# Performance work log

Hardware: AMD Instinct MI355X
Metric: run time of the kernel (lower is better)

## Reference

```python
import jax, jax.numpy as jnp
import numpy as np

NUM_GROUPS = 32
EPS = 1e-6


def group_norm(x, gamma, beta):
    # x: [b, c, h, w]
    b, c, h, w = x.shape
    xg = x.reshape(b, NUM_GROUPS, c // NUM_GROUPS, h, w)
    mean = jnp.mean(xg, axis=(2, 3, 4), keepdims=True)
    var = jnp.var(xg, axis=(2, 3, 4), keepdims=True)
    xn = ((xg - mean) * jax.lax.rsqrt(var + EPS)).reshape(b, c, h, w)
    return xn * gamma[None, :, None, None] + beta[None, :, None, None]


def conv1x1(x, w, b):
    # 1x1 conv == channel-mixing linear: x [b,c,h,w], w [o,c], b [o]
    return jnp.einsum('bchw,oc->bohw', x, w) + b[None, :, None, None]


def setup_inputs() -> dict:
    key = jax.random.key(0)
    ks = jax.random.split(key, 11)
    B, C, H, W = 4, 512, 64, 64
    scale = 1.0 / np.sqrt(C)
    inp = {
        'x': jax.random.normal(ks[0], (B, C, H, W), jnp.float32),
        'gn_gamma': jnp.ones((C,), jnp.float32),
        'gn_beta': jnp.zeros((C,), jnp.float32),
        'wq': jax.random.normal(ks[1], (C, C), jnp.float32) * scale,
        'bq': jnp.zeros((C,), jnp.float32),
        'wk': jax.random.normal(ks[2], (C, C), jnp.float32) * scale,
        'bk': jnp.zeros((C,), jnp.float32),
        'wv': jax.random.normal(ks[3], (C, C), jnp.float32) * scale,
        'bv': jnp.zeros((C,), jnp.float32),
        'wo': jax.random.normal(ks[4], (C, C), jnp.float32) * scale,
        'bo': jnp.zeros((C,), jnp.float32),
    }
    return inp


def reference(x, gn_gamma, gn_beta, wq, bq, wk, bk, wv, bv, wo, bo):
    b, c, h, w = x.shape
    nx = group_norm(x, gn_gamma, gn_beta)
    q = conv1x1(nx, wq, bq).reshape(b, c, h * w)
    k = conv1x1(nx, wk, bk).reshape(b, c, h * w)
    v = conv1x1(nx, wv, bv).reshape(b, c, h * w)
    # score[b, i, j] = <q[:, i], k[:, j]> / sqrt(c); softmax over j (keys)
    score = jnp.einsum('bci,bcj->bij', q, k) / jnp.sqrt(jnp.asarray(c, x.dtype))
    score = jax.nn.softmax(score, axis=2)
    # out[b, c, i] = sum_j v[b, c, j] * score[b, i, j]
    out = jnp.einsum('bcj,bij->bci', v, score).reshape(b, c, h, w)
    out = conv1x1(out, wo, bo)
    return x + out
```

## Files before the change

### kernel.cpp

```cpp
#include <hip/hip_runtime.h>

#define B_   4
#define C_   512
#define G_   32
#define CPG  16
#define N_   4096

typedef unsigned short u16;
typedef __attribute__((ext_vector_type(4))) float f32x4;
typedef __attribute__((ext_vector_type(8))) short s16x8;
typedef __attribute__((ext_vector_type(8))) u16   u16x8;
typedef __attribute__((ext_vector_type(4))) u16   u16x4;

__device__ __forceinline__ u16 f2bf(float f) {
    union { float f; unsigned u; } x; x.f = f;
    unsigned r = x.u + 0x7fffu + ((x.u >> 16) & 1u);
    return (u16)(r >> 16);
}

__global__ __launch_bounds__(256)
void gn_stats_kernel(const float* __restrict__ x,
                     const float* __restrict__ gamma,
                     const float* __restrict__ beta,
                     float* __restrict__ scale,
                     float* __restrict__ shift)
{
    int bg = blockIdx.x;
    int b = bg >> 5, g = bg & 31;
    const float* base = x + (size_t)(b * C_ + g * CPG) * N_;
    const int nelem = CPG * N_;
    int t = threadIdx.x;

    float s = 0.f, ss = 0.f;
    for (int i = t * 4; i < nelem; i += 256 * 4) {
        float4 v = *reinterpret_cast<const float4*>(base + i);
        s  += v.x + v.y + v.z + v.w;
        ss += v.x * v.x + v.y * v.y + v.z * v.z + v.w * v.w;
    }
    __shared__ float rs[256], rss[256];
    rs[t] = s; rss[t] = ss;
    __syncthreads();
    for (int off = 128; off > 0; off >>= 1) {
        if (t < off) { rs[t] += rs[t + off]; rss[t] += rss[t + off]; }
        __syncthreads();
    }
    __shared__ float mean_s, rstd_s;
    if (t == 0) {
        float mean = rs[0] / (float)nelem;
        float var  = rss[0] / (float)nelem - mean * mean;
        mean_s = mean;
        rstd_s = rsqrtf(var + 1e-6f);
    }
    __syncthreads();
    if (t < CPG) {
        int c = g * CPG + t;
        float sc = gamma[c] * rstd_s;
        scale[b * C_ + c] = sc;
        shift[b * C_ + c] = beta[c] - mean_s * sc;
    }
}

__global__ __launch_bounds__(256)
void wcvt_kernel(const float* __restrict__ wq, const float* __restrict__ wk,
                 const float* __restrict__ wv, const float* __restrict__ wo,
                 u16* __restrict__ wqb, u16* __restrict__ wkb,
                 u16* __restrict__ wvb, u16* __restrict__ wob)
{
    int idx = (blockIdx.x * 256 + threadIdx.x) * 4;
    {
        float4 a = *reinterpret_cast<const float4*>(wq + idx);
        u16x4 r = { f2bf(a.x), f2bf(a.y), f2bf(a.z), f2bf(a.w) };
        *reinterpret_cast<u16x4*>(wqb + idx) = r;
    }
    {
        float4 a = *reinterpret_cast<const float4*>(wk + idx);
        u16x4 r = { f2bf(a.x), f2bf(a.y), f2bf(a.z), f2bf(a.w) };
        *reinterpret_cast<u16x4*>(wkb + idx) = r;
    }
    {
        float4 a = *reinterpret_cast<const float4*>(wv + idx);
        u16x4 r = { f2bf(a.x), f2bf(a.y), f2bf(a.z), f2bf(a.w) };
        *reinterpret_cast<u16x4*>(wvb + idx) = r;
    }
    {
        float4 a = *reinterpret_cast<const float4*>(wo + idx);
        u16x4 r = { f2bf(a.x), f2bf(a.y), f2bf(a.z), f2bf(a.w) };
        *reinterpret_cast<u16x4*>(wob + idx) = r;
    }
}

__global__ __launch_bounds__(256)
void nxt_kernel(const float* __restrict__ x, const float* __restrict__ scale,
                const float* __restrict__ shift, u16* __restrict__ nx_t)
{
    int b  = blockIdx.z;
    int n0 = blockIdx.x * 64, c0 = blockIdx.y * 64;
    const float* xb = x + ((size_t)b * C_ + c0) * N_ + n0;
    u16* ob = nx_t + ((size_t)b * N_ + n0) * C_ + c0;
    int t = threadIdx.x;
    int tx = t & 15, ty = t >> 4;

    __shared__ float tile[64][65];
    #pragma unroll
    for (int r = 0; r < 4; ++r) {
        int c = ty * 4 + r;
        float sc = scale[b * C_ + c0 + c];
        float sh = shift[b * C_ + c0 + c];
        float4 v = *reinterpret_cast<const float4*>(xb + (size_t)c * N_ + tx * 4);
        tile[c][tx * 4 + 0] = v.x * sc + sh;
        tile[c][tx * 4 + 1] = v.y * sc + sh;
        tile[c][tx * 4 + 2] = v.z * sc + sh;
        tile[c][tx * 4 + 3] = v.w * sc + sh;
    }
    __syncthreads();
    int nn = t >> 2, cc0 = (t & 3) * 16;
    u16x8 o0, o1;
    #pragma unroll
    for (int j = 0; j < 8; ++j) o0[j] = f2bf(tile[cc0 + j][nn]);
    #pragma unroll
    for (int j = 0; j < 8; ++j) o1[j] = f2bf(tile[cc0 + 8 + j][nn]);
    *reinterpret_cast<u16x8*>(ob + (size_t)nn * C_ + cc0)     = o0;
    *reinterpret_cast<u16x8*>(ob + (size_t)nn * C_ + cc0 + 8) = o1;
}

template<int BM, int BN, int EPI>
__device__ __forceinline__
void gemm_dev(int i0, int j0,
              const u16* __restrict__ A, const u16* __restrict__ B,
              void* __restrict__ Dp, const float* __restrict__ bias,
              const float* __restrict__ resid,
              int Nn, int K, int lda, int ldb, float scl,
              const float* __restrict__ colsc)
{
    constexpr int WM = BM / 2, WN = BN / 2;
    constexpr int MI = WM / 16, NI = WN / 16;

    __shared__ u16 As[BM * 64];
    __shared__ u16 Bs[BN * 64];

    const int t  = threadIdx.x;
    const int l  = t & 63;
    const int w  = t >> 6;
    const int wr = w >> 1;
    const int wc = w & 1;

    const int srow = l >> 3;
    const int sgr  = ((l & 7) ^ (l >> 3)) * 8;

    const int fr = l & 15;
    const int q  = l >> 4;

    f32x4 acc[MI][NI];
    #pragma unroll
    for (int a = 0; a < MI; ++a)
        #pragma unroll
        for (int b2 = 0; b2 < NI; ++b2) acc[a][b2] = 0.f;

    for (int k0 = 0; k0 < K; k0 += 64) {
        #pragma unroll
        for (int r = 0; r < BM / 32; ++r) {
            int s = r * 4 + w;
            const u16* ga = A + (size_t)(i0 + s * 8 + srow) * lda + (k0 + sgr);
            __builtin_amdgcn_global_load_lds(
                (const __attribute__((address_space(1))) void*)ga,
                (__attribute__((address_space(3))) void*)&As[s * 512], 16, 0, 0);
        }
        #pragma unroll
        for (int r = 0; r < BN / 32; ++r) {
            int s = r * 4 + w;
            const u16* gb = B + (size_t)(j0 + s * 8 + srow) * ldb + (k0 + sgr);
            __builtin_amdgcn_global_load_lds(
                (const __attribute__((address_space(1))) void*)gb,
                (__attribute__((address_space(3))) void*)&Bs[s * 512], 16, 0, 0);
        }
        __syncthreads();

        #pragma unroll
        for (int h = 0; h < 2; ++h) {
            s16x8 af[MI], bfr[NI];
            #pragma unroll
            for (int mi = 0; mi < MI; ++mi) {
                int r = wr * WM + mi * 16 + fr;
                int p = (h * 4 + q) ^ (r & 7);
                af[mi] = *reinterpret_cast<const s16x8*>(&As[r * 64 + p * 8]);
            }
            #pragma unroll
            for (int ni = 0; ni < NI; ++ni) {
                int r = wc * WN + ni * 16 + fr;
                int p = (h * 4 + q) ^ (r & 7);
                bfr[ni] = *reinterpret_cast<const s16x8*>(&Bs[r * 64 + p * 8]);
            }
            #pragma unroll
            for (int mi = 0; mi < MI; ++mi)
                #pragma unroll
                for (int ni = 0; ni < NI; ++ni)
                    acc[mi][ni] = __builtin_amdgcn_mfma_f32_16x16x32_bf16(
                        af[mi], bfr[ni], acc[mi][ni], 0, 0, 0);
        }
        __syncthreads();
    }

    const int orow = (l >> 4) * 4;
    const int ocol = l & 15;

    if constexpr (EPI == 2) {
        u16* D = (u16*)Dp;
        #pragma unroll
        for (int mi = 0; mi < MI; ++mi) {
            int ib = i0 + wr * WM + mi * 16 + orow;
            #pragma unroll
            for (int ni = 0; ni < NI; ++ni) {
                int jb = j0 + wc * WN + ni * 16 + ocol;
                #pragma unroll
                for (int e = 0; e < 4; ++e)
                    D[(size_t)(ib + e) * Nn + jb] =
                        f2bf(__expf(acc[mi][ni][e] * scl));
            }
        }
    } else {
        #pragma unroll
        for (int mi = 0; mi < MI; ++mi) {
            #pragma unroll
            for (int ni = 0; ni < NI; ++ni) {
                int ib = i0 + wr * WM + mi * 16 + orow;
                int jb = j0 + wc * WN + ni * 16 + ocol;
                if constexpr (EPI == 0 || EPI == 1 || EPI == 4) {
                    u16* D = (u16*)Dp;
                    float bj = 0.f;
                    if constexpr (EPI == 0) bj = bias[jb];
                    #pragma unroll
                    for (int e = 0; e < 4; ++e) {
                        float vv = acc[mi][ni][e];
                        if constexpr (EPI == 0) vv += bj;
                        if constexpr (EPI == 1) vv += bias[ib + e];
                        D[(size_t)(ib + e) * Nn + jb] = f2bf(vv);
                    }
                } else {
                    float* D = (float*)Dp;
                    float cs = colsc[jb];
                    #pragma unroll
                    for (int e = 0; e < 4; ++e)
                        D[(size_t)(ib + e) * Nn + jb] =
                            acc[mi][ni][e] * cs + bias[ib + e] + resid[(size_t)(ib + e) * Nn + jb];
                }
            }
        }
    }
}

__global__ __launch_bounds__(256)
void qk_gemm(const u16* __restrict__ nx_t, const u16* __restrict__ wqb,
             const u16* __restrict__ wkb, const float* __restrict__ bq,
             const float* __restrict__ bk, u16* __restrict__ q_t,
             u16* __restrict__ k_t)
{
    int z = blockIdx.z, b = z & 3, isk = z >> 2;
    gemm_dev<128, 128, 0>(blockIdx.y * 128, blockIdx.x * 128,
                          nx_t + (size_t)b * N_ * C_, isk ? wkb : wqb,
                          (isk ? k_t : q_t) + (size_t)b * N_ * C_,
                          isk ? bk : bq, nullptr, C_, C_, C_, C_, 1.f, nullptr);
}

__global__ __launch_bounds__(256)
void v_gemm(const u16* __restrict__ wvb, const u16* __restrict__ nx_t,
            const float* __restrict__ bv, u16* __restrict__ vbuf)
{
    int b = blockIdx.z;
    gemm_dev<128, 128, 1>(blockIdx.y * 128, blockIdx.x * 128,
                          wvb, nx_t + (size_t)b * N_ * C_, vbuf + (size_t)b * C_ * N_,
                          bv, nullptr, N_, C_, C_, C_, 1.f, nullptr);
}

__global__ __launch_bounds__(256)
void scores_gemm(const u16* __restrict__ q_t, const u16* __restrict__ k_t,
                 u16* __restrict__ S_bf)
{
    int b = blockIdx.z;
    gemm_dev<128, 128, 2>(blockIdx.y * 128, blockIdx.x * 128,
                          q_t + (size_t)b * N_ * C_, k_t + (size_t)b * N_ * C_,
                          S_bf + (size_t)b * N_ * N_, nullptr, nullptr, N_, C_, C_, C_,
                          0.044194173824159216f, nullptr);
}

__global__ __launch_bounds__(256)
void lsum_kernel(const u16* __restrict__ S_bf, float* __restrict__ inv_l)
{
    int row = blockIdx.x * 4 + (threadIdx.x >> 6);
    int lane = threadIdx.x & 63;
    const u16* p = S_bf + (size_t)row * N_ + lane * 8;
    float s = 0.f;
    #pragma unroll
    for (int it = 0; it < 8; ++it) {
        u16x8 v = *reinterpret_cast<const u16x8*>(p + it * 512);
        #pragma unroll
        for (int j = 0; j < 8; ++j) {
            union { unsigned u; float f; } cv; cv.u = (unsigned)v[j] << 16;
            s += cv.f;
        }
    }
    #pragma unroll
    for (int m2 = 1; m2 < 64; m2 <<= 1) s += __shfl_xor(s, m2);
    if (lane == 0) inv_l[row] = 1.f / s;
}

__global__ __launch_bounds__(256)
void pv_part(const u16* __restrict__ S_bf, const u16* __restrict__ vbuf,
             u16* __restrict__ attn_t)
{
    int id  = blockIdx.x;
    int xcd = id & 7, slot = id >> 3;
    int yz  = xcd * 16 + (slot >> 3);
    int ct  = slot & 7;
    int it  = yz & 31, b = yz >> 5;
    const u16* Pb = S_bf + (size_t)b * N_ * N_;
    const u16* Vb = vbuf + (size_t)b * C_ * N_;
    u16*       Ob = attn_t + (size_t)b * N_ * C_;

    const int i0 = it * 128, c0 = ct * 64;
    const int t = threadIdx.x, l = t & 63, w = t >> 6;
    const int wr = w >> 1, wc = w & 1;
    const int srow = l >> 3;
    const int sgr  = ((l & 7) ^ (l >> 3)) * 8;
    const int fr = l & 15, q = l >> 4;

    __shared__ u16 As[128 * 64];
    __shared__ u16 Bs[64 * 64];

    f32x4 acc[4][2];
    #pragma unroll
    for (int a = 0; a < 4; ++a)
        #pragma unroll
        for (int b2 = 0; b2 < 2; ++b2) acc[a][b2] = 0.f;

    for (int k0 = 0; k0 < N_; k0 += 64) {
        #pragma unroll
        for (int r = 0; r < 4; ++r) {
            int s = r * 4 + w;
            const u16* ga = Pb + (size_t)(i0 + s * 8 + srow) * N_ + (k0 + sgr);
            __builtin_amdgcn_global_load_lds(
                (const __attribute__((address_space(1))) void*)ga,
                (__attribute__((address_space(3))) void*)&As[s * 512], 16, 0, 0);
        }
        #pragma unroll
        for (int r = 0; r < 2; ++r) {
            int s = r * 4 + w;
            const u16* gb = Vb + (size_t)(c0 + s * 8 + srow) * N_ + (k0 + sgr);
            __builtin_amdgcn_global_load_lds(
                (const __attribute__((address_space(1))) void*)gb,
                (__attribute__((address_space(3))) void*)&Bs[s * 512], 16, 0, 0);
        }
        __syncthreads();
        #pragma unroll
        for (int h = 0; h < 2; ++h) {
            s16x8 af[4], bfr[2];
            #pragma unroll
            for (int mi = 0; mi < 4; ++mi) {
                int r = wr * 64 + mi * 16 + fr;
                int p = (h * 4 + q) ^ (r & 7);
                af[mi] = *reinterpret_cast<const s16x8*>(&As[r * 64 + p * 8]);
            }
            #pragma unroll
            for (int ni = 0; ni < 2; ++ni) {
                int r = wc * 32 + ni * 16 + fr;
                int p = (h * 4 + q) ^ (r & 7);
                bfr[ni] = *reinterpret_cast<const s16x8*>(&Bs[r * 64 + p * 8]);
            }
            #pragma unroll
            for (int mi = 0; mi < 4; ++mi)
                #pragma unroll
                for (int ni = 0; ni < 2; ++ni)
                    acc[mi][ni] = __builtin_amdgcn_mfma_f32_16x16x32_bf16(
                        af[mi], bfr[ni], acc[mi][ni], 0, 0, 0);
        }
        __syncthreads();
    }

    const int orow = (l >> 4) * 4;
    const int ocol = l & 15;
    #pragma unroll
    for (int mi = 0; mi < 4; ++mi) {
        #pragma unroll
        for (int ni = 0; ni < 2; ++ni) {
            int ib = i0 + wr * 64 + mi * 16 + orow;
            int jb = c0 + wc * 32 + ni * 16 + ocol;
            #pragma unroll
            for (int e = 0; e < 4; ++e)
                Ob[(size_t)(ib + e) * C_ + jb] = f2bf(acc[mi][ni][e]);
        }
    }
}

__global__ __launch_bounds__(256)
void final_gemm(const u16* __restrict__ wob, const u16* __restrict__ attn_t,
                const float* __restrict__ bo, const float* __restrict__ x,
                const float* __restrict__ inv_l, float* __restrict__ outp)
{
    int b = blockIdx.z;
    gemm_dev<128, 128, 3>(blockIdx.y * 128, blockIdx.x * 128,
                          wob, attn_t + (size_t)b * N_ * C_, outp + (size_t)b * C_ * N_,
                          bo, x + (size_t)b * C_ * N_, N_, C_, C_, C_, 1.f,
                          inv_l + (size_t)b * N_);
}

extern "C" void kernel_launch(void* const* d_in, const int* in_sizes, int n_in,
                              void* d_out, int out_size, void* d_ws, size_t ws_size,
                              hipStream_t stream)
{
    const float* x     = (const float*)d_in[0];
    const float* gamma = (const float*)d_in[1];
    const float* beta  = (const float*)d_in[2];
    const float* wq    = (const float*)d_in[3];
    const float* bq    = (const float*)d_in[4];
    const float* wk    = (const float*)d_in[5];
    const float* bk    = (const float*)d_in[6];
    const float* wv    = (const float*)d_in[7];
    const float* bv    = (const float*)d_in[8];
    const float* wo    = (const float*)d_in[9];
    const float* bo    = (const float*)d_in[10];
    float* out = (float*)d_out;

    char* p = (char*)d_ws;
    auto take = [&](size_t bytes) { char* r = p; p += (bytes + 255) & ~(size_t)255; return r; };
    float* scale = (float*)take(B_ * C_ * 4);
    float* shift = (float*)take(B_ * C_ * 4);
    u16* wqb = (u16*)take((size_t)C_ * C_ * 2);
    u16* wkb = (u16*)take((size_t)C_ * C_ * 2);
    u16* wvb = (u16*)take((size_t)C_ * C_ * 2);
    u16* wob = (u16*)take((size_t)C_ * C_ * 2);
    u16* nx_t  = (u16*)take((size_t)B_ * N_ * C_ * 2);
    u16* q_t   = (u16*)take((size_t)B_ * N_ * C_ * 2);
    u16* k_t   = (u16*)take((size_t)B_ * N_ * C_ * 2);
    u16* vbuf  = (u16*)take((size_t)B_ * C_ * N_ * 2);
    float* inv_l = (float*)take((size_t)B_ * N_ * 4);
    u16* S_bf = (u16*)take((size_t)B_ * N_ * N_ * 2);
    u16* attn_t = nx_t;

    gn_stats_kernel<<<128, 256, 0, stream>>>(x, gamma, beta, scale, shift);
    wcvt_kernel<<<256, 256, 0, stream>>>(wq, wk, wv, wo, wqb, wkb, wvb, wob);
    nxt_kernel<<<dim3(N_ / 64, C_ / 64, B_), 256, 0, stream>>>(x, scale, shift, nx_t);

    qk_gemm<<<dim3(C_ / 128, N_ / 128, 8), 256, 0, stream>>>(nx_t, wqb, wkb, bq, bk, q_t, k_t);
    v_gemm<<<dim3(N_ / 128, C_ / 128, B_), 256, 0, stream>>>(wvb, nx_t, bv, vbuf);

    scores_gemm<<<dim3(N_ / 128, N_ / 128, B_), 256, 0, stream>>>(q_t, k_t, S_bf);
    lsum_kernel<<<B_ * N_ / 4, 256, 0, stream>>>(S_bf, inv_l);
    pv_part<<<1024, 256, 0, stream>>>(S_bf, vbuf, attn_t);

    final_gemm<<<dim3(N_ / 128, C_ / 128, B_), 256, 0, stream>>>(wob, attn_t, bo, x, inv_l, out);
}
```

Before: 285.5 us.

## Fuse softmax row-sum into PV kernel and remap scores grid per XCD

Removes the separate row-sum kernel, which re-read the whole bf16 score matrix. The first channel-tile block of each PV row group now sums the A fragments it already loads and writes the row sums, and the final GEMM takes their reciprocal. The scores GEMM also moves to a 1D grid whose block ids are grouped by XCD, so blocks on the same die share Q/K tiles in L2. The added summation runs only in ct==0 blocks, which may slow those blocks and unbalance work across the grid.

```diff
diff --git a/kernel.cpp b/kernel.cpp
--- a/kernel.cpp
+++ b/kernel.cpp
@@ -237,7 +237,7 @@
                     }
                 } else {
                     float* D = (float*)Dp;
-                    float cs = colsc[jb];
+                    float cs = 1.f / colsc[jb];
                     #pragma unroll
                     for (int e = 0; e < 4; ++e)
                         D[(size_t)(ib + e) * Nn + jb] =
@@ -275,37 +275,20 @@
 void scores_gemm(const u16* __restrict__ q_t, const u16* __restrict__ k_t,
                  u16* __restrict__ S_bf)
 {
-    int b = blockIdx.z;
-    gemm_dev<128, 128, 2>(blockIdx.y * 128, blockIdx.x * 128,
+    int id   = blockIdx.x;
+    int xcd  = id & 7, slot = id >> 3;
+    int jt   = slot & 31;
+    int gidx = xcd * 16 + (slot >> 5);
+    int it   = gidx & 31, b = gidx >> 5;
+    gemm_dev<128, 128, 2>(it * 128, jt * 128,
                           q_t + (size_t)b * N_ * C_, k_t + (size_t)b * N_ * C_,
                           S_bf + (size_t)b * N_ * N_, nullptr, nullptr, N_, C_, C_, C_,
                           0.044194173824159216f, nullptr);
 }
 
 __global__ __launch_bounds__(256)
-void lsum_kernel(const u16* __restrict__ S_bf, float* __restrict__ inv_l)
-{
-    int row = blockIdx.x * 4 + (threadIdx.x >> 6);
-    int lane = threadIdx.x & 63;
-    const u16* p = S_bf + (size_t)row * N_ + lane * 8;
-    float s = 0.f;
-    #pragma unroll
-    for (int it = 0; it < 8; ++it) {
-        u16x8 v = *reinterpret_cast<const u16x8*>(p + it * 512);
-        #pragma unroll
-        for (int j = 0; j < 8; ++j) {
-            union { unsigned u; float f; } cv; cv.u = (unsigned)v[j] << 16;
-            s += cv.f;
-        }
-    }
-    #pragma unroll
-    for (int m2 = 1; m2 < 64; m2 <<= 1) s += __shfl_xor(s, m2);
-    if (lane == 0) inv_l[row] = 1.f / s;
-}
-
-__global__ __launch_bounds__(256)
 void pv_part(const u16* __restrict__ S_bf, const u16* __restrict__ vbuf,
-             u16* __restrict__ attn_t)
+             u16* __restrict__ attn_t, float* __restrict__ lbuf)
 {
     int id  = blockIdx.x;
     int xcd = id & 7, slot = id >> 3;
@@ -332,6 +315,8 @@
         #pragma unroll
         for (int b2 = 0; b2 < 2; ++b2) acc[a][b2] = 0.f;
 
+    float rsum[4] = {0.f, 0.f, 0.f, 0.f};
+
     for (int k0 = 0; k0 < N_; k0 += 64) {
         #pragma unroll
         for (int r = 0; r < 4; ++r) {
@@ -365,6 +350,19 @@
                 int p = (h * 4 + q) ^ (r & 7);
                 bfr[ni] = *reinterpret_cast<const s16x8*>(&Bs[r * 64 + p * 8]);
             }
+            if (ct == 0) {
+                #pragma unroll
+                for (int mi = 0; mi < 4; ++mi) {
+                    float s = 0.f;
+                    #pragma unroll
+                    for (int j = 0; j < 8; ++j) {
+                        union { unsigned u; float f; } cv;
+                        cv.u = (unsigned)(u16)af[mi][j] << 16;
+                        s += cv.f;
+                    }
+                    rsum[mi] += s;
+                }
+            }
             #pragma unroll
             for (int mi = 0; mi < 4; ++mi)
                 #pragma unroll
@@ -375,6 +373,19 @@
         __syncthreads();
     }
 
+    if (ct == 0) {
+        #pragma unroll
+        for (int mi = 0; mi < 4; ++mi) {
+            rsum[mi] += __shfl_xor(rsum[mi], 16);
+            rsum[mi] += __shfl_xor(rsum[mi], 32);
+        }
+        if (wc == 0 && l < 16) {
+            #pragma unroll
+            for (int mi = 0; mi < 4; ++mi)
+                lbuf[(size_t)b * N_ + i0 + wr * 64 + mi * 16 + l] = rsum[mi];
+        }
+    }
+
     const int orow = (l >> 4) * 4;
     const int ocol = l & 15;
     #pragma unroll
@@ -393,13 +404,13 @@
 __global__ __launch_bounds__(256)
 void final_gemm(const u16* __restrict__ wob, const u16* __restrict__ attn_t,
                 const float* __restrict__ bo, const float* __restrict__ x,
-                const float* __restrict__ inv_l, float* __restrict__ outp)
+                const float* __restrict__ lbuf, float* __restrict__ outp)
 {
     int b = blockIdx.z;
     gemm_dev<128, 128, 3>(blockIdx.y * 128, blockIdx.x * 128,
                           wob, attn_t + (size_t)b * N_ * C_, outp + (size_t)b * C_ * N_,
                           bo, x + (size_t)b * C_ * N_, N_, C_, C_, C_, 1.f,
-                          inv_l + (size_t)b * N_);
+                          lbuf + (size_t)b * N_);
 }
 
 extern "C" void kernel_launch(void* const* d_in, const int* in_sizes, int n_in,
@@ -431,7 +442,7 @@
     u16* q_t   = (u16*)take((size_t)B_ * N_ * C_ * 2);
     u16* k_t   = (u16*)take((size_t)B_ * N_ * C_ * 2);
     u16* vbuf  = (u16*)take((size_t)B_ * C_ * N_ * 2);
-    float* inv_l = (float*)take((size_t)B_ * N_ * 4);
+    float* lbuf = (float*)take((size_t)B_ * N_ * 4);
     u16* S_bf = (u16*)take((size_t)B_ * N_ * N_ * 2);
     u16* attn_t = nx_t;
 
@@ -442,9 +453,8 @@
     qk_gemm<<<dim3(C_ / 128, N_ / 128, 8), 256, 0, stream>>>(nx_t, wqb, wkb, bq, bk, q_t, k_t);
     v_gemm<<<dim3(N_ / 128, C_ / 128, B_), 256, 0, stream>>>(wvb, nx_t, bv, vbuf);
 
-    scores_gemm<<<dim3(N_ / 128, N_ / 128, B_), 256, 0, stream>>>(q_t, k_t, S_bf);
-    lsum_kernel<<<B_ * N_ / 4, 256, 0, stream>>>(S_bf, inv_l);
-    pv_part<<<1024, 256, 0, stream>>>(S_bf, vbuf, attn_t);
-
-    final_gemm<<<dim3(N_ / 128, C_ / 128, B_), 256, 0, stream>>>(wob, attn_t, bo, x, inv_l, out);
-}
+    scores_gemm<<<4096, 256, 0, stream>>>(q_t, k_t, S_bf);
+    pv_part<<<1024, 256, 0, stream>>>(S_bf, vbuf, attn_t, lbuf);
+
+    final_gemm<<<dim3(N_ / 128, C_ / 128, B_), 256, 0, stream>>>(wob, attn_t, bo, x, lbuf, out);
+}
```

After: 310.5 us. +8.8%, slower.
